# Optimization experiments

Measured on AMD Instinct MI355X. Metric: run time of the kernel, lower is better.

## Reference

```python
import jax, jax.numpy as jnp
import numpy as np

ZERO = -1e4  # Semiring.zero (finite log-zero, as in the torch repo)


def semiring_eye(n, dtype=jnp.float32):
    # log-semiring identity: 0 on diagonal, ZERO off-diagonal
    return jnp.where(jnp.eye(n, dtype=bool), jnp.zeros((), dtype), jnp.full((), ZERO, dtype))


def log_bmm(a, b):
    # LogSemiring.bmm: out[..., i, j] = logsumexp_k(a[..., i, k] + b[..., k, j])
    # matmul-based stable form: avoids materializing the [..., i, k, j] tensor
    am = jnp.max(a, axis=-1, keepdims=True)          # [..., i, 1]
    bm = jnp.max(b, axis=-2, keepdims=True)          # [..., 1, j]
    return am + bm + jnp.log(jnp.matmul(jnp.exp(a - am), jnp.exp(b - bm)))


def crf_reduce(potentials):
    # tree-doubling scan, faithful to reduce() in the torch source
    B, L, T, _ = potentials.shape
    n = L.bit_length()
    pad = (1 << n) - L
    eye = jnp.broadcast_to(semiring_eye(T, potentials.dtype), (B, pad, T, T))
    p = jnp.concatenate([potentials, eye], axis=1)
    for _ in range(n):
        p = log_bmm(p[:, 0::2], p[:, 1::2])
    return p[:, 0]  # [B, T, T]


def setup_inputs() -> dict:
    key = jax.random.key(0)
    k1, k2, k3, k4 = jax.random.split(key, 4)
    B, L, T = 32, 1024, 64
    logits = jax.random.normal(k1, (B, L, T), jnp.float32)
    mask = jnp.ones((B, L), dtype=bool)
    # xavier_normal_ for square matrix: std = sqrt(2 / (T + T))
    transitions = jax.random.normal(k2, (T, T), jnp.float32) * np.sqrt(2.0 / (T + T)).astype(np.float32)
    start_states = jax.random.normal(k3, (T,), jnp.float32)
    end_states = jax.random.normal(k4, (T,), jnp.float32)
    return {"logits": logits, "transitions": transitions,
            "start_states": start_states, "end_states": end_states, "mask": mask}


def reference(logits, transitions, start_states, end_states, mask):
    B, L, T = logits.shape
    end_idx = jnp.sum(mask, axis=-1) - 1                      # [B]
    # include_start: add start_states to first step
    logits = logits.at[:, 0].add(start_states)
    # include_end: scatter-add end_states at last unmasked step
    logits = logits.at[jnp.arange(B), end_idx].add(end_states)
    # zero out padded positions
    logits = logits * mask[..., None]
    me = mask[:, 1:, None, None]                              # [B, L-1, 1, 1]
    trans = transitions[None, None] * me                      # [B, L-1, T, T]
    # LogSemiring.mul == add
    pot = logits[:, 1:, None, :] + trans                      # [B, L-1, T, T]
    pot = pot * me + semiring_eye(T, logits.dtype) * (~me)
    red = crf_reduce(pot)                                     # [B, T, T]
    red = red + logits[:, 0][..., None]                       # start_potentials[..., None]
    return jax.nn.logsumexp(red, axis=(-1, -2))               # [B] log-partition
```

## Files before the change

### kernel.cpp

```cpp
#include <hip/hip_runtime.h>
#include <hip/hip_bf16.h>

typedef __attribute__((ext_vector_type(8))) short short8;
typedef __attribute__((ext_vector_type(4))) float floatx4;
typedef __attribute__((ext_vector_type(4))) unsigned int uint4v;
typedef __attribute__((ext_vector_type(2))) unsigned int uint2v;

#define L_SEQ    1024
#define N_BATCH  32
#define CHUNKA   32
#define NCHUNKA  32
#define REC_SH   4096
#define MST      72

__device__ __forceinline__ unsigned short f2bf(float f) {
    unsigned u = __builtin_bit_cast(unsigned, f);
    return (unsigned short)((u + 0x8000u) >> 16);
}
__device__ __forceinline__ float bf2f(unsigned short h) {
    return __builtin_bit_cast(float, ((unsigned)h) << 16);
}
__device__ __forceinline__ unsigned pkbf(float hi, float lo) {
    unsigned uh = __builtin_bit_cast(unsigned, hi) + 0x8000u;
    unsigned ul = __builtin_bit_cast(unsigned, lo) + 0x8000u;
    return __builtin_amdgcn_perm(uh, ul, 0x07060302u);
}

__device__ __forceinline__ void gload_lds16(const void* g, void* l) {
    __builtin_amdgcn_global_load_lds(
        (const __attribute__((address_space(1))) void*)g,
        (__attribute__((address_space(3))) void*)l, 16, 0, 0);
}

__device__ __forceinline__ int rec_idx(int n, int u) {
    return n * 64 + (u ^ (n & 7)) * 8;
}

#define MFMA16(A, B, C) __builtin_amdgcn_mfma_f32_16x16x32_bf16((A), (B), (C), 0, 0, 0)

__global__ __launch_bounds__(256, 4) void crf_phaseA(
    const float* __restrict__ logits, const float* __restrict__ trans,
    const float* __restrict__ end_states, unsigned short* __restrict__ wsA,
    float* __restrict__ sclA)
{
    __shared__ __align__(16) unsigned short Me[64 * MST];
    __shared__ __align__(16) float LdsE[CHUNKA * 64];
    __shared__ float offs[4];

    const int tid = threadIdx.x, lane = tid & 63, w = tid >> 6;
    const int q = lane >> 4, c = lane & 15, R0 = w * 16;
    const int b = blockIdx.y, chunk = blockIdx.x;

    {
        short8 z = {0, 0, 0, 0, 0, 0, 0, 0};
        for (int idx = tid; idx < 64 * MST / 8; idx += 256)
            ((short8*)Me)[idx] = z;
    }
    __syncthreads();
    if (tid < 64) Me[tid * MST + tid] = 0x3F80;

    const int l0 = 1 + chunk * CHUNKA;
    const int lend = (l0 + CHUNKA < L_SEQ) ? (l0 + CHUNKA) : L_SEQ;
    const int stageBase = l0 - ((chunk == NCHUNKA - 1) ? 1 : 0);

    {
        const float* gsrc = logits + (size_t)b * L_SEQ * 64 + (size_t)stageBase * 64;
        #pragma unroll
        for (int i = 0; i < 2; ++i) {
            const int ch = 2 * w + i;
            gload_lds16(gsrc + ch * 256 + lane * 4, &LdsE[ch * 256]);
        }
    }

    short8 bfr[4][2];
    #pragma unroll
    for (int t = 0; t < 4; ++t) {
        #pragma unroll
        for (int h = 0; h < 2; ++h) {
            short8 v;
            #pragma unroll
            for (int j = 0; j < 8; ++j)
                v[j] = (short)f2bf(__expf(trans[(h * 32 + q * 8 + j) * 64 + t * 16 + c]));
            bfr[t][h] = v;
        }
    }
    __syncthreads();

    for (int i = tid; i < CHUNKA * 64 / 4; i += 256) {
        floatx4 v = ((floatx4*)LdsE)[i];
        if (stageBase + (i >> 4) == L_SEQ - 1) {
            const int j0 = (i & 15) * 4;
            #pragma unroll
            for (int e = 0; e < 4; ++e) v[e] += end_states[j0 + e];
        }
        #pragma unroll
        for (int e = 0; e < 4; ++e) v[e] = __expf(v[e]);
        ((floatx4*)LdsE)[i] = v;
    }
    __syncthreads();

    float off = 0.f;
    const unsigned short* brow = &Me[(R0 + c) * MST + q * 8];
    unsigned short* wrow = &Me[(R0 + c) * MST];

    for (int l = l0; l < lend; ++l) {
        const int s = l - l0;
        const bool renorm = ((s & 7) == 7) || (l == lend - 1);
        const int li = l - stageBase;

        floatx4 ewv[4];
        #pragma unroll
        for (int t = 0; t < 4; ++t)
            ewv[t] = *(const floatx4*)&LdsE[li * 64 + t * 16 + q * 4];

        short8 b0 = *(const short8*)brow;
        short8 b1 = *(const short8*)(brow + 32);

        float h[4][4];
        #pragma unroll
        for (int t = 0; t < 4; ++t) {
            floatx4 z = {0.f, 0.f, 0.f, 0.f};
            z = MFMA16(bfr[t][0], b0, z);
            z = MFMA16(bfr[t][1], b1, z);
            #pragma unroll
            for (int r = 0; r < 4; ++r) h[t][r] = z[r] * ewv[t][r];
        }

        if (renorm) {
            float m = h[0][0];
            #pragma unroll
            for (int t = 0; t < 4; ++t)
                #pragma unroll
                for (int r = 0; r < 4; ++r) m = fmaxf(m, h[t][r]);
            #pragma unroll
            for (int d = 32; d >= 1; d >>= 1) m = fmaxf(m, __shfl_xor(m, d, 64));
            m = fmaxf(m, 1e-30f);
            float inv = __builtin_amdgcn_rcpf(m);
            off += __logf(m);
            #pragma unroll
            for (int t = 0; t < 4; ++t)
                #pragma unroll
                for (int r = 0; r < 4; ++r) h[t][r] *= inv;
        }

        #pragma unroll
        for (int t = 0; t < 4; ++t) {
            uint2v d;
            d[0] = pkbf(h[t][1], h[t][0]);
            d[1] = pkbf(h[t][3], h[t][2]);
            *(uint2v*)(wrow + t * 16 + q * 4) = d;
        }
    }

    if (lane == 0) offs[w] = off;
    __syncthreads();

    float omax = fmaxf(fmaxf(offs[0], offs[1]), fmaxf(offs[2], offs[3]));
    const int rid = b * NCHUNKA + chunk;
    unsigned short* rec = wsA + (size_t)rid * REC_SH;
    const int n = tid & 63, qq = tid >> 6;
    float eo = __expf(offs[qq] - omax);
    unsigned short tmp[16] __attribute__((aligned(16)));
    #pragma unroll
    for (int r = 0; r < 16; ++r)
        tmp[r] = f2bf(bf2f(Me[(qq * 16 + r) * MST + n]) * eo);
    *(uint4v*)(rec + rec_idx(n, 2 * qq))     = *(uint4v*)(tmp);
    *(uint4v*)(rec + rec_idx(n, 2 * qq + 1)) = *(uint4v*)(tmp + 8);
    if (tid == 0) sclA[rid] = omax;
}

template<int NSTEPS, bool FINAL>
__global__ __launch_bounds__(256) void crf_combine(
    const unsigned short* __restrict__ inRecs, const float* __restrict__ sclIn,
    unsigned short* __restrict__ outRecs, float* __restrict__ sclOut,
    const float* __restrict__ logits, const float* __restrict__ start_states,
    float* __restrict__ out)
{
    __shared__ __align__(16) unsigned short Me[64 * MST];
    __shared__ __align__(16) unsigned short stageb[2][REC_SH];
    __shared__ float offs[4];
    __shared__ float es[64];
    __shared__ float redA;
    __shared__ float wsum[4];

    const int tid = threadIdx.x, lane = tid & 63, w = tid >> 6;
    const int q = lane >> 4, c = lane & 15, R0 = w * 16;
    const int b = blockIdx.y, g = blockIdx.x;
    const int recBase = (b * gridDim.x + g) * NSTEPS;

    {
        short8 z = {0, 0, 0, 0, 0, 0, 0, 0};
        for (int idx = tid; idx < 64 * MST / 8; idx += 256)
            ((short8*)Me)[idx] = z;
    }
    __syncthreads();
    if (tid < 64) Me[tid * MST + tid] = 0x3F80;

    float sstep[NSTEPS];
    #pragma unroll
    for (int s = 0; s < NSTEPS; ++s) sstep[s] = sclIn[recBase + s];

    auto stage = [&](int s, int buf) {
        const unsigned short* src = inRecs + (size_t)(recBase + s) * REC_SH;
        #pragma unroll
        for (int i = 0; i < 2; ++i) {
            const int ch = 2 * w + i;
            gload_lds16(src + ch * 512 + lane * 8, &stageb[buf][ch * 512]);
        }
    };
    stage(0, 0);
    __syncthreads();

    float off = 0.f;
    const unsigned short* brow = &Me[(R0 + c) * MST + q * 8];
    unsigned short* wrow = &Me[(R0 + c) * MST];

    #pragma unroll
    for (int s = 0; s < NSTEPS; ++s) {
        if (s + 1 < NSTEPS) stage(s + 1, (s + 1) & 1);
        const unsigned short* buf = stageb[s & 1];
        off += sstep[s];

        short8 b0 = *(const short8*)brow;
        short8 b1 = *(const short8*)(brow + 32);

        float h[4][4];
        #pragma unroll
        for (int t = 0; t < 4; ++t) {
            const int n = t * 16 + c;
            short8 a0 = *(const short8*)(buf + rec_idx(n, 0 * 4 + q));
            short8 a1 = *(const short8*)(buf + rec_idx(n, 1 * 4 + q));
            floatx4 z = {0.f, 0.f, 0.f, 0.f};
            z = MFMA16(a0, b0, z);
            z = MFMA16(a1, b1, z);
            #pragma unroll
            for (int r = 0; r < 4; ++r) h[t][r] = z[r];
        }

        if (!FINAL && s == NSTEPS - 1) {
            float m = h[0][0];
            #pragma unroll
            for (int t = 0; t < 4; ++t)
                #pragma unroll
                for (int r = 0; r < 4; ++r) m = fmaxf(m, h[t][r]);
            #pragma unroll
            for (int d = 32; d >= 1; d >>= 1) m = fmaxf(m, __shfl_xor(m, d, 64));
            m = fmaxf(m, 1e-30f);
            float inv = __builtin_amdgcn_rcpf(m);
            off += __logf(m);
            #pragma unroll
            for (int t = 0; t < 4; ++t)
                #pragma unroll
                for (int r = 0; r < 4; ++r) h[t][r] *= inv;
        }

        #pragma unroll
        for (int t = 0; t < 4; ++t) {
            uint2v d;
            d[0] = pkbf(h[t][1], h[t][0]);
            d[1] = pkbf(h[t][3], h[t][2]);
            *(uint2v*)(wrow + t * 16 + q * 4) = d;
        }
        __syncthreads();
    }

    if (lane == 0) offs[w] = off;
    __syncthreads();

    if (!FINAL) {
        float omax = fmaxf(fmaxf(offs[0], offs[1]), fmaxf(offs[2], offs[3]));
        const int oid = b * gridDim.x + g;
        unsigned short* rec = outRecs + (size_t)oid * REC_SH;
        const int n = tid & 63, qq = tid >> 6;
        float eo = __expf(offs[qq] - omax);
        unsigned short tmp[16] __attribute__((aligned(16)));
        #pragma unroll
        for (int r = 0; r < 16; ++r)
            tmp[r] = f2bf(bf2f(Me[(qq * 16 + r) * MST + n]) * eo);
        *(uint4v*)(rec + rec_idx(n, 2 * qq))     = *(uint4v*)(tmp);
        *(uint4v*)(rec + rec_idx(n, 2 * qq + 1)) = *(uint4v*)(tmp + 8);
        if (tid == 0) sclOut[oid] = omax;
    } else {
        if (w == 0) {
            float u = offs[lane >> 4] + logits[(size_t)b * L_SEQ * 64 + lane]
                      + start_states[lane];
            float A1 = u;
            #pragma unroll
            for (int d = 32; d >= 1; d >>= 1) A1 = fmaxf(A1, __shfl_xor(A1, d, 64));
            es[lane] = __expf(u - A1);
            if (lane == 0) redA = A1;
        }
        __syncthreads();
        const int i = tid >> 2, jb = (tid & 3) * 16;
        float sum = 0.f;
        #pragma unroll
        for (int j = 0; j < 16; ++j) sum += bf2f(Me[i * MST + jb + j]);
        sum *= es[i];
        #pragma unroll
        for (int d = 32; d >= 1; d >>= 1) sum += __shfl_xor(sum, d, 64);
        if (lane == 0) wsum[w] = sum;
        __syncthreads();
        if (tid == 0)
            out[b] = redA + __logf(wsum[0] + wsum[1] + wsum[2] + wsum[3]);
    }
}

extern "C" void kernel_launch(void* const* d_in, const int* in_sizes, int n_in,
                              void* d_out, int out_size, void* d_ws, size_t ws_size,
                              hipStream_t stream)
{
    const float* logits       = (const float*)d_in[0];
    const float* trans        = (const float*)d_in[1];
    const float* start_states = (const float*)d_in[2];
    const float* end_states   = (const float*)d_in[3];

    unsigned short* wsA = (unsigned short*)d_ws;
    unsigned short* wsB = wsA + (size_t)N_BATCH * NCHUNKA * REC_SH;
    float* sclA = (float*)(wsB + (size_t)N_BATCH * 4 * REC_SH);
    float* sclB = sclA + N_BATCH * NCHUNKA;
    float* out  = (float*)d_out;

    crf_phaseA<<<dim3(NCHUNKA, N_BATCH), 256, 0, stream>>>(
        logits, trans, end_states, wsA, sclA);
    crf_combine<8, false><<<dim3(4, N_BATCH), 256, 0, stream>>>(
        wsA, sclA, wsB, sclB, nullptr, nullptr, nullptr);
    crf_combine<4, true><<<dim3(1, N_BATCH), 256, 0, stream>>>(
        wsB, sclB, nullptr, nullptr, logits, start_states, out);
}
```

Measured before the change: 99.51 us.

## Merge two combine stages into one kernel with register-prefetched records

Replaces the two-level combine (8-step then 4-step kernels) with a single final kernel per batch that chains all 32 chunk records in sequence. Records are prefetched three steps ahead straight from global memory into registers instead of being staged through LDS, and the per-step barrier is dropped. Renormalisation now runs every 8 steps. Phase A's step loop is also unrolled in groups of 8 with renormalisation decided at compile time. This removes one kernel launch and the intermediate workspace round trip, at the cost of a longer serial chain per block on only 32 blocks and heavier register use.

```diff
diff --git a/kernel.cpp b/kernel.cpp
--- a/kernel.cpp
+++ b/kernel.cpp
@@ -103,11 +103,7 @@
     const unsigned short* brow = &Me[(R0 + c) * MST + q * 8];
     unsigned short* wrow = &Me[(R0 + c) * MST];
 
-    for (int l = l0; l < lend; ++l) {
-        const int s = l - l0;
-        const bool renorm = ((s & 7) == 7) || (l == lend - 1);
-        const int li = l - stageBase;
-
+    auto stepf = [&](int li, bool renorm) {
         floatx4 ewv[4];
         #pragma unroll
         for (int t = 0; t < 4; ++t)
@@ -150,6 +146,18 @@
             d[1] = pkbf(h[t][3], h[t][2]);
             *(uint2v*)(wrow + t * 16 + q * 4) = d;
         }
+    };
+
+    if (chunk != NCHUNKA - 1) {
+        const int liBase = l0 - stageBase;
+        for (int g = 0; g < 4; ++g) {
+            #pragma unroll
+            for (int k = 0; k < 8; ++k)
+                stepf(liBase + g * 8 + k, k == 7);
+        }
+    } else {
+        for (int s = 0; s < 31; ++s)
+            stepf(l0 - stageBase + s, ((s & 7) == 7) || (s == 30));
     }
 
     if (lane == 0) offs[w] = off;
@@ -169,15 +177,12 @@
     if (tid == 0) sclA[rid] = omax;
 }
 
-template<int NSTEPS, bool FINAL>
-__global__ __launch_bounds__(256) void crf_combine(
-    const unsigned short* __restrict__ inRecs, const float* __restrict__ sclIn,
-    unsigned short* __restrict__ outRecs, float* __restrict__ sclOut,
+__global__ __launch_bounds__(256) void crf_final(
+    const unsigned short* __restrict__ recs, const float* __restrict__ sclIn,
     const float* __restrict__ logits, const float* __restrict__ start_states,
     float* __restrict__ out)
 {
     __shared__ __align__(16) unsigned short Me[64 * MST];
-    __shared__ __align__(16) unsigned short stageb[2][REC_SH];
     __shared__ float offs[4];
     __shared__ float es[64];
     __shared__ float redA;
@@ -185,8 +190,8 @@
 
     const int tid = threadIdx.x, lane = tid & 63, w = tid >> 6;
     const int q = lane >> 4, c = lane & 15, R0 = w * 16;
-    const int b = blockIdx.y, g = blockIdx.x;
-    const int recBase = (b * gridDim.x + g) * NSTEPS;
+    const int b = blockIdx.x;
+    const unsigned short* base = recs + (size_t)b * NCHUNKA * REC_SH;
 
     {
         short8 z = {0, 0, 0, 0, 0, 0, 0, 0};
@@ -195,31 +200,31 @@
     }
     __syncthreads();
     if (tid < 64) Me[tid * MST + tid] = 0x3F80;
-
-    float sstep[NSTEPS];
-    #pragma unroll
-    for (int s = 0; s < NSTEPS; ++s) sstep[s] = sclIn[recBase + s];
-
-    auto stage = [&](int s, int buf) {
-        const unsigned short* src = inRecs + (size_t)(recBase + s) * REC_SH;
-        #pragma unroll
-        for (int i = 0; i < 2; ++i) {
-            const int ch = 2 * w + i;
-            gload_lds16(src + ch * 512 + lane * 8, &stageb[buf][ch * 512]);
-        }
-    };
-    stage(0, 0);
-    __syncthreads();
-
-    float off = 0.f;
+    __syncthreads();
+
     const unsigned short* brow = &Me[(R0 + c) * MST + q * 8];
     unsigned short* wrow = &Me[(R0 + c) * MST];
 
-    #pragma unroll
-    for (int s = 0; s < NSTEPS; ++s) {
-        if (s + 1 < NSTEPS) stage(s + 1, (s + 1) & 1);
-        const unsigned short* buf = stageb[s & 1];
-        off += sstep[s];
+    auto loadA = [&](int s, short8 A[4][2]) {
+        const unsigned short* r = base + (size_t)s * REC_SH;
+        #pragma unroll
+        for (int t = 0; t < 4; ++t) {
+            const int n = t * 16 + c;
+            A[t][0] = *(const short8*)(r + rec_idx(n, q));
+            A[t][1] = *(const short8*)(r + rec_idx(n, 4 + q));
+        }
+    };
+
+    short8 A[3][4][2];
+    loadA(0, A[0]);
+    loadA(1, A[1]);
+    loadA(2, A[2]);
+
+    float off = 0.f;
+    #pragma unroll
+    for (int s = 0; s < NCHUNKA; ++s) {
+        const int cs = s % 3;
+        off += sclIn[b * NCHUNKA + s];
 
         short8 b0 = *(const short8*)brow;
         short8 b1 = *(const short8*)(brow + 32);
@@ -227,17 +232,14 @@
         float h[4][4];
         #pragma unroll
         for (int t = 0; t < 4; ++t) {
-            const int n = t * 16 + c;
-            short8 a0 = *(const short8*)(buf + rec_idx(n, 0 * 4 + q));
-            short8 a1 = *(const short8*)(buf + rec_idx(n, 1 * 4 + q));
             floatx4 z = {0.f, 0.f, 0.f, 0.f};
-            z = MFMA16(a0, b0, z);
-            z = MFMA16(a1, b1, z);
+            z = MFMA16(A[cs][t][0], b0, z);
+            z = MFMA16(A[cs][t][1], b1, z);
             #pragma unroll
             for (int r = 0; r < 4; ++r) h[t][r] = z[r];
         }
 
-        if (!FINAL && s == NSTEPS - 1) {
+        if ((s & 7) == 7) {
             float m = h[0][0];
             #pragma unroll
             for (int t = 0; t < 4; ++t)
@@ -261,48 +263,34 @@
             d[1] = pkbf(h[t][3], h[t][2]);
             *(uint2v*)(wrow + t * 16 + q * 4) = d;
         }
-        __syncthreads();
+
+        if (s + 3 < NCHUNKA) loadA(s + 3, A[cs]);
     }
 
     if (lane == 0) offs[w] = off;
     __syncthreads();
 
-    if (!FINAL) {
-        float omax = fmaxf(fmaxf(offs[0], offs[1]), fmaxf(offs[2], offs[3]));
-        const int oid = b * gridDim.x + g;
-        unsigned short* rec = outRecs + (size_t)oid * REC_SH;
-        const int n = tid & 63, qq = tid >> 6;
-        float eo = __expf(offs[qq] - omax);
-        unsigned short tmp[16] __attribute__((aligned(16)));
-        #pragma unroll
-        for (int r = 0; r < 16; ++r)
-            tmp[r] = f2bf(bf2f(Me[(qq * 16 + r) * MST + n]) * eo);
-        *(uint4v*)(rec + rec_idx(n, 2 * qq))     = *(uint4v*)(tmp);
-        *(uint4v*)(rec + rec_idx(n, 2 * qq + 1)) = *(uint4v*)(tmp + 8);
-        if (tid == 0) sclOut[oid] = omax;
-    } else {
-        if (w == 0) {
-            float u = offs[lane >> 4] + logits[(size_t)b * L_SEQ * 64 + lane]
-                      + start_states[lane];
-            float A1 = u;
-            #pragma unroll
-            for (int d = 32; d >= 1; d >>= 1) A1 = fmaxf(A1, __shfl_xor(A1, d, 64));
-            es[lane] = __expf(u - A1);
-            if (lane == 0) redA = A1;
-        }
-        __syncthreads();
-        const int i = tid >> 2, jb = (tid & 3) * 16;
-        float sum = 0.f;
-        #pragma unroll
-        for (int j = 0; j < 16; ++j) sum += bf2f(Me[i * MST + jb + j]);
-        sum *= es[i];
-        #pragma unroll
-        for (int d = 32; d >= 1; d >>= 1) sum += __shfl_xor(sum, d, 64);
-        if (lane == 0) wsum[w] = sum;
-        __syncthreads();
-        if (tid == 0)
-            out[b] = redA + __logf(wsum[0] + wsum[1] + wsum[2] + wsum[3]);
-    }
+    if (w == 0) {
+        float u = offs[lane >> 4] + logits[(size_t)b * L_SEQ * 64 + lane]
+                  + start_states[lane];
+        float A1 = u;
+        #pragma unroll
+        for (int d = 32; d >= 1; d >>= 1) A1 = fmaxf(A1, __shfl_xor(A1, d, 64));
+        es[lane] = __expf(u - A1);
+        if (lane == 0) redA = A1;
+    }
+    __syncthreads();
+    const int i = tid >> 2, jb = (tid & 3) * 16;
+    float sum = 0.f;
+    #pragma unroll
+    for (int j = 0; j < 16; ++j) sum += bf2f(Me[i * MST + jb + j]);
+    sum *= es[i];
+    #pragma unroll
+    for (int d = 32; d >= 1; d >>= 1) sum += __shfl_xor(sum, d, 64);
+    if (lane == 0) wsum[w] = sum;
+    __syncthreads();
+    if (tid == 0)
+        out[b] = redA + __logf(wsum[0] + wsum[1] + wsum[2] + wsum[3]);
 }
 
 extern "C" void kernel_launch(void* const* d_in, const int* in_sizes, int n_in,
@@ -315,15 +303,11 @@
     const float* end_states   = (const float*)d_in[3];
 
     unsigned short* wsA = (unsigned short*)d_ws;
-    unsigned short* wsB = wsA + (size_t)N_BATCH * NCHUNKA * REC_SH;
-    float* sclA = (float*)(wsB + (size_t)N_BATCH * 4 * REC_SH);
-    float* sclB = sclA + N_BATCH * NCHUNKA;
+    float* sclA = (float*)(wsA + (size_t)N_BATCH * NCHUNKA * REC_SH);
     float* out  = (float*)d_out;
 
     crf_phaseA<<<dim3(NCHUNKA, N_BATCH), 256, 0, stream>>>(
         logits, trans, end_states, wsA, sclA);
-    crf_combine<8, false><<<dim3(4, N_BATCH), 256, 0, stream>>>(
-        wsA, sclA, wsB, sclB, nullptr, nullptr, nullptr);
-    crf_combine<4, true><<<dim3(1, N_BATCH), 256, 0, stream>>>(
-        wsB, sclB, nullptr, nullptr, logits, start_states, out);
-}
+    crf_final<<<N_BATCH, 256, 0, stream>>>(
+        wsA, sclA, logits, start_states, out);
+}
```

Result: slower. 112.0 us (+12.6%).

## Keep chunk running product in registers instead of LDS round-trip per step

Applied to the files above, without the earlier changes.

Each step's MFMA output is now repacked straight into the B-operand registers for the next step. To make this possible, the k-index permutation of the transition A fragments is changed so the output layout lines up with the operand layout. This removes the per-step LDS write and read of the state matrix and the identity initialization of LDS. It also unrolls the inner loop by 8 with static renormalization. The cost is more register pressure and reliance on the MFMA output/input layout correspondence being exactly right.

```diff
diff --git a/kernel.cpp b/kernel.cpp
--- a/kernel.cpp
+++ b/kernel.cpp
@@ -51,14 +51,6 @@
     const int q = lane >> 4, c = lane & 15, R0 = w * 16;
     const int b = blockIdx.y, chunk = blockIdx.x;
 
-    {
-        short8 z = {0, 0, 0, 0, 0, 0, 0, 0};
-        for (int idx = tid; idx < 64 * MST / 8; idx += 256)
-            ((short8*)Me)[idx] = z;
-    }
-    __syncthreads();
-    if (tid < 64) Me[tid * MST + tid] = 0x3F80;
-
     const int l0 = 1 + chunk * CHUNKA;
     const int lend = (l0 + CHUNKA < L_SEQ) ? (l0 + CHUNKA) : L_SEQ;
     const int stageBase = l0 - ((chunk == NCHUNKA - 1) ? 1 : 0);
@@ -79,8 +71,10 @@
         for (int h = 0; h < 2; ++h) {
             short8 v;
             #pragma unroll
-            for (int j = 0; j < 8; ++j)
-                v[j] = (short)f2bf(__expf(trans[(h * 32 + q * 8 + j) * 64 + t * 16 + c]));
+            for (int j = 0; j < 8; ++j) {
+                const int kk = (2 * h + (j >> 2)) * 16 + q * 4 + (j & 3);
+                v[j] = (short)f2bf(__expf(trans[kk * 64 + t * 16 + c]));
+            }
             bfr[t][h] = v;
         }
     }
@@ -99,22 +93,27 @@
     }
     __syncthreads();
 
+    unsigned P[8];
+    #pragma unroll
+    for (int t = 0; t < 4; ++t) {
+        float h0 = (t * 16 + q * 4 + 0 == R0 + c) ? 1.f : 0.f;
+        float h1 = (t * 16 + q * 4 + 1 == R0 + c) ? 1.f : 0.f;
+        float h2 = (t * 16 + q * 4 + 2 == R0 + c) ? 1.f : 0.f;
+        float h3 = (t * 16 + q * 4 + 3 == R0 + c) ? 1.f : 0.f;
+        P[2 * t]     = pkbf(h1, h0);
+        P[2 * t + 1] = pkbf(h3, h2);
+    }
+
     float off = 0.f;
-    const unsigned short* brow = &Me[(R0 + c) * MST + q * 8];
-    unsigned short* wrow = &Me[(R0 + c) * MST];
-
-    for (int l = l0; l < lend; ++l) {
-        const int s = l - l0;
-        const bool renorm = ((s & 7) == 7) || (l == lend - 1);
-        const int li = l - stageBase;
-
+
+    auto stepf = [&](int li, bool renorm) {
         floatx4 ewv[4];
         #pragma unroll
         for (int t = 0; t < 4; ++t)
             ewv[t] = *(const floatx4*)&LdsE[li * 64 + t * 16 + q * 4];
 
-        short8 b0 = *(const short8*)brow;
-        short8 b1 = *(const short8*)(brow + 32);
+        const short8 b0 = __builtin_bit_cast(short8, (uint4v){P[0], P[1], P[2], P[3]});
+        const short8 b1 = __builtin_bit_cast(short8, (uint4v){P[4], P[5], P[6], P[7]});
 
         float h[4][4];
         #pragma unroll
@@ -145,13 +144,31 @@
 
         #pragma unroll
         for (int t = 0; t < 4; ++t) {
-            uint2v d;
-            d[0] = pkbf(h[t][1], h[t][0]);
-            d[1] = pkbf(h[t][3], h[t][2]);
+            P[2 * t]     = pkbf(h[t][1], h[t][0]);
+            P[2 * t + 1] = pkbf(h[t][3], h[t][2]);
+        }
+    };
+
+    if (chunk != NCHUNKA - 1) {
+        const int liBase = l0 - stageBase;
+        for (int g = 0; g < 4; ++g) {
+            #pragma unroll
+            for (int k = 0; k < 8; ++k)
+                stepf(liBase + g * 8 + k, k == 7);
+        }
+    } else {
+        for (int s = 0; s < 31; ++s)
+            stepf(l0 - stageBase + s, ((s & 7) == 7) || (s == 30));
+    }
+
+    {
+        unsigned short* wrow = &Me[(R0 + c) * MST];
+        #pragma unroll
+        for (int t = 0; t < 4; ++t) {
+            uint2v d = {P[2 * t], P[2 * t + 1]};
             *(uint2v*)(wrow + t * 16 + q * 4) = d;
         }
     }
-
     if (lane == 0) offs[w] = off;
     __syncthreads();
 
```

New measurement: 96.96 us. -2.6%, faster.
